# Kernel optimization log

Hardware: AMD Instinct MI355X
Metric: run time of the kernel (lower is better)

Reference implementation:

```python
import jax, jax.numpy as jnp
import numpy as np

N_ENTITIES = 100000
N_RELATIONS = 100
EMB = 64         # entity embedding_size
REL_DIM = 64     # relation_dim
BATCH = 65536


def setup_inputs() -> dict:
    key = jax.random.key(0)
    k1, k2, k3, k4, k5, k6 = jax.random.split(key, 6)
    head = jax.random.randint(k1, (BATCH,), 0, N_ENTITIES)
    relation = jax.random.randint(k2, (BATCH,), 0, N_RELATIONS)
    tail = jax.random.randint(k3, (BATCH,), 0, N_ENTITIES)
    entity_emb = jax.random.normal(k4, (N_ENTITIES, EMB), dtype=jnp.float32)
    relation_emb = jax.random.normal(k5, (N_RELATIONS, REL_DIM), dtype=jnp.float32)
    proj_emb = jax.random.normal(k6, (N_RELATIONS, EMB * REL_DIM), dtype=jnp.float32)
    return {
        "head": head,
        "relation": relation,
        "tail": tail,
        "entity_emb": entity_emb,
        "relation_emb": relation_emb,
        "proj_emb": proj_emb,
    }


def reference(head, relation, tail, entity_emb, relation_emb, proj_emb):
    h_emb = entity_emb[head]                           # [B, E]
    t_emb = entity_emb[tail]                           # [B, E]
    r_emb = relation_emb[relation]                     # [B, R]
    proj = proj_emb[relation].reshape(-1, EMB, REL_DIM)  # [B, E, R]
    h_proj = jnp.einsum('be,ber->br', h_emb, proj)     # [B, R]
    t_proj = jnp.einsum('be,ber->br', t_emb, proj)     # [B, R]
    diff = h_proj + r_emb - t_proj
    score = jnp.sum(diff * diff, axis=1)               # [B]
    return score
```

## Files before the change

kernel.cpp:

```cpp
#include <hip/hip_runtime.h>

#define BATCH   65536
#define NREL    100
#define NBB     64
#define NTILE   16

typedef __attribute__((ext_vector_type(8))) short bf16x8;
typedef __attribute__((ext_vector_type(4))) float f32x4;

__device__ __forceinline__ unsigned short f2bf(float x) {
    unsigned u = __float_as_uint(x);
    u += 0x7fffu + ((u >> 16) & 1u);
    return (unsigned short)(u >> 16);
}

__launch_bounds__(256)
__global__ void transr_bucket(const int* __restrict__ relation,
                              int* __restrict__ ws_hist,
                              int* __restrict__ ws_lpfx,
                              int* __restrict__ ws_bucket) {
    __shared__ int hist[NREL];
    __shared__ int scan[128];
    const int tid = threadIdx.x, bid = blockIdx.x;

    for (int r = tid; r < NREL; r += 256) hist[r] = 0;
    __syncthreads();

    const int4 v = ((const int4*)relation)[bid * 256 + tid];
    const int vals[4] = {v.x, v.y, v.z, v.w};
    int lr[4];
    #pragma unroll
    for (int k = 0; k < 4; ++k) lr[k] = atomicAdd(&hist[vals[k]], 1);
    __syncthreads();

    if (tid < 128) scan[tid] = (tid < NREL) ? hist[tid] : 0;
    __syncthreads();
    #pragma unroll
    for (int off = 1; off < 128; off <<= 1) {
        int t = 0;
        if (tid < 128 && tid >= off) t = scan[tid - off];
        __syncthreads();
        if (tid < 128) scan[tid] += t;
        __syncthreads();
    }

    const int i0 = (bid * 256 + tid) * 4;
    #pragma unroll
    for (int k = 0; k < 4; ++k) {
        const int rel = vals[k];
        ws_bucket[bid * 1024 + (scan[rel] - hist[rel]) + lr[k]] = i0 + k;
    }
    for (int r = tid; r < NREL; r += 256) {
        ws_hist[r * NBB + bid] = hist[r];
        ws_lpfx[r * NBB + bid] = scan[r] - hist[r];
    }
}

__launch_bounds__(256)
__global__ void transr_compute(const int* __restrict__ head,
                               const int* __restrict__ tail,
                               const float* __restrict__ ent,
                               const float* __restrict__ remb,
                               const float* __restrict__ proj,
                               const int* __restrict__ ws_hist,
                               const int* __restrict__ ws_lpfx,
                               const int* __restrict__ ws_bucket,
                               float* __restrict__ out) {
    __shared__ unsigned short Abuf[64 * 64];
    __shared__ unsigned short Bbuf[64 * 64];
    __shared__ float remb_s[64];
    __shared__ int   pfx_s[64];
    __shared__ int   lpfx_s[64];
    __shared__ int   bidx_s[64];
    __shared__ int   cnt_s;

    const int tid   = threadIdx.x;
    const int wid   = tid >> 6;
    const int lane  = tid & 63;
    const int rel   = blockIdx.y;
    const int start = blockIdx.x << 6;

    if (wid == 0) {
        int h = ws_hist[rel * NBB + lane];
        lpfx_s[lane] = ws_lpfx[rel * NBB + lane];
        const int own = h;
        #pragma unroll
        for (int m = 1; m < 64; m <<= 1) {
            int t = __shfl_up(h, m);
            if (lane >= m) h += t;
        }
        pfx_s[lane] = h - own;
        if (lane == 63) cnt_s = h;
    }

    {
        const int k = tid >> 2, q = tid & 3;
        const float4* p4 = (const float4*)(proj + (size_t)rel * 4096 + k * 64 + q * 16);
        const int khi = k >> 3, klo = k & 7;
        #pragma unroll
        for (int m = 0; m < 4; ++m) {
            float4 v = p4[m];
            const float vv[4] = {v.x, v.y, v.z, v.w};
            #pragma unroll
            for (int j2 = 0; j2 < 4; ++j2) {
                const int n = q * 16 + m * 4 + j2;
                Bbuf[n * 64 + ((khi ^ (n & 7)) * 8) + klo] = f2bf(vv[j2]);
            }
        }
    }
    if (tid < 64) remb_s[tid] = remb[rel * 64 + tid];
    __syncthreads();

    const int cnt = cnt_s;
    if (start >= cnt) return;

    {
        const int row = tid >> 2, q = tid & 3;
        const int j  = start + row;
        const int jj = (j < cnt) ? j : (cnt - 1);
        int lo = 0;
        #pragma unroll
        for (int s = 32; s; s >>= 1) {
            const int c = lo + s;
            if (c < 64 && pfx_s[c] <= jj) lo = c;
        }
        const int b = ws_bucket[lo * 1024 + lpfx_s[lo] + (jj - pfx_s[lo])];
        if (q == 0) bidx_s[row] = b;
        const int h = head[b], t = tail[b];
        const float4* h4 = (const float4*)(ent + (size_t)h * 64) + q * 4;
        const float4* t4 = (const float4*)(ent + (size_t)t * 64) + q * 4;
        #pragma unroll
        for (int i = 0; i < 2; ++i) {
            unsigned short u[8];
            #pragma unroll
            for (int m = 0; m < 2; ++m) {
                float4 a = h4[i * 2 + m], c = t4[i * 2 + m];
                u[m * 4 + 0] = f2bf(a.x - c.x);
                u[m * 4 + 1] = f2bf(a.y - c.y);
                u[m * 4 + 2] = f2bf(a.z - c.z);
                u[m * 4 + 3] = f2bf(a.w - c.w);
            }
            const int slice = (q * 2 + i) ^ (row & 7);
            *(bf16x8*)&Abuf[row * 64 + slice * 8] = *(bf16x8*)u;
        }
    }
    __syncthreads();

    const int arow = wid * 16 + (lane & 15);
    const int g    = lane >> 4;

    f32x4 acc[4];
    #pragma unroll
    for (int f = 0; f < 4; ++f) {
        const float rv = remb_s[f * 16 + (lane & 15)];
        acc[f] = (f32x4){rv, rv, rv, rv};
    }
    #pragma unroll
    for (int s = 0; s < 2; ++s) {
        const int ks = g + s * 4;
        bf16x8 av = *(const bf16x8*)&Abuf[arow * 64 + ((ks ^ (arow & 7)) * 8)];
        #pragma unroll
        for (int f = 0; f < 4; ++f) {
            const int col = f * 16 + (lane & 15);
            bf16x8 bv = *(const bf16x8*)&Bbuf[col * 64 + ((ks ^ (col & 7)) * 8)];
            acc[f] = __builtin_amdgcn_mfma_f32_16x16x32_bf16(av, bv, acc[f], 0, 0, 0);
        }
    }

    float ps[4];
    #pragma unroll
    for (int r = 0; r < 4; ++r)
        ps[r] = acc[0][r] * acc[0][r] + acc[1][r] * acc[1][r] +
                acc[2][r] * acc[2][r] + acc[3][r] * acc[3][r];
    #pragma unroll
    for (int m = 1; m < 16; m <<= 1) {
        #pragma unroll
        for (int r = 0; r < 4; ++r) ps[r] += __shfl_xor(ps[r], m, 64);
    }
    if ((lane & 15) == 0) {
        const int rowb = wid * 16 + g * 4;
        #pragma unroll
        for (int r = 0; r < 4; ++r) {
            const int j = start + rowb + r;
            if (j < cnt) out[bidx_s[rowb + r]] = ps[r];
        }
    }
}

extern "C" void kernel_launch(void* const* d_in, const int* in_sizes, int n_in,
                              void* d_out, int out_size, void* d_ws, size_t ws_size,
                              hipStream_t stream) {
    const int*   head     = (const int*)d_in[0];
    const int*   relation = (const int*)d_in[1];
    const int*   tail     = (const int*)d_in[2];
    const float* ent      = (const float*)d_in[3];
    const float* remb     = (const float*)d_in[4];
    const float* proj     = (const float*)d_in[5];
    float*       out      = (float*)d_out;

    int* ws_hist   = (int*)d_ws;
    int* ws_lpfx   = (int*)d_ws + 8192;
    int* ws_bucket = (int*)d_ws + 16384;

    transr_bucket<<<NBB, 256, 0, stream>>>(relation, ws_hist, ws_lpfx, ws_bucket);
    transr_compute<<<dim3(NTILE, NREL), 256, 0, stream>>>(
        head, tail, ent, remb, proj, ws_hist, ws_lpfx, ws_bucket, out);
}
```

Before: 22.72 us.

## Precompute bf16 swizzled projection matrices in prep kernel, copy into LDS in compute

```diff
diff --git a/kernel.cpp b/kernel.cpp
--- a/kernel.cpp
+++ b/kernel.cpp
@@ -15,44 +15,63 @@
 }
 
 __launch_bounds__(256)
-__global__ void transr_bucket(const int* __restrict__ relation,
-                              int* __restrict__ ws_hist,
-                              int* __restrict__ ws_lpfx,
-                              int* __restrict__ ws_bucket) {
-    __shared__ int hist[NREL];
-    __shared__ int scan[128];
+__global__ void transr_prep(const int* __restrict__ relation,
+                            const float* __restrict__ proj,
+                            int* __restrict__ ws_hist,
+                            int* __restrict__ ws_lpfx,
+                            int* __restrict__ ws_bucket,
+                            unsigned short* __restrict__ ws_pbf) {
     const int tid = threadIdx.x, bid = blockIdx.x;
 
-    for (int r = tid; r < NREL; r += 256) hist[r] = 0;
-    __syncthreads();
-
-    const int4 v = ((const int4*)relation)[bid * 256 + tid];
-    const int vals[4] = {v.x, v.y, v.z, v.w};
-    int lr[4];
-    #pragma unroll
-    for (int k = 0; k < 4; ++k) lr[k] = atomicAdd(&hist[vals[k]], 1);
-    __syncthreads();
-
-    if (tid < 128) scan[tid] = (tid < NREL) ? hist[tid] : 0;
-    __syncthreads();
-    #pragma unroll
-    for (int off = 1; off < 128; off <<= 1) {
-        int t = 0;
-        if (tid < 128 && tid >= off) t = scan[tid - off];
+    if (bid < NBB) {
+        __shared__ int hist[NREL];
+        __shared__ int scan[128];
+
+        for (int r = tid; r < NREL; r += 256) hist[r] = 0;
         __syncthreads();
-        if (tid < 128) scan[tid] += t;
+
+        const int4 v = ((const int4*)relation)[bid * 256 + tid];
+        const int vals[4] = {v.x, v.y, v.z, v.w};
+        int lr[4];
+        #pragma unroll
+        for (int k = 0; k < 4; ++k) lr[k] = atomicAdd(&hist[vals[k]], 1);
         __syncthreads();
-    }
-
-    const int i0 = (bid * 256 + tid) * 4;
-    #pragma unroll
-    for (int k = 0; k < 4; ++k) {
-        const int rel = vals[k];
-        ws_bucket[bid * 1024 + (scan[rel] - hist[rel]) + lr[k]] = i0 + k;
-    }
-    for (int r = tid; r < NREL; r += 256) {
-        ws_hist[r * NBB + bid] = hist[r];
-        ws_lpfx[r * NBB + bid] = scan[r] - hist[r];
+
+        if (tid < 128) scan[tid] = (tid < NREL) ? hist[tid] : 0;
+        __syncthreads();
+        #pragma unroll
+        for (int off = 1; off < 128; off <<= 1) {
+            int t = 0;
+            if (tid < 128 && tid >= off) t = scan[tid - off];
+            __syncthreads();
+            if (tid < 128) scan[tid] += t;
+            __syncthreads();
+        }
+
+        const int i0 = (bid * 256 + tid) * 4;
+        #pragma unroll
+        for (int k = 0; k < 4; ++k) {
+            const int rel = vals[k];
+            ws_bucket[bid * 1024 + (scan[rel] - hist[rel]) + lr[k]] = i0 + k;
+        }
+        for (int r = tid; r < NREL; r += 256) {
+            ws_hist[r * NBB + bid] = hist[r];
+            ws_lpfx[r * NBB + bid] = scan[r] - hist[r];
+        }
+    } else {
+        const int rel = bid - NBB;
+        const int n = tid >> 2, q = tid & 3;
+        const float* Pr = proj + (size_t)rel * 4096;
+        unsigned short* dst = ws_pbf + (size_t)rel * 4096;
+        #pragma unroll
+        for (int kh = 0; kh < 2; ++kh) {
+            const int khi = q * 2 + kh;
+            unsigned short u[8];
+            #pragma unroll
+            for (int klo = 0; klo < 8; ++klo)
+                u[klo] = f2bf(Pr[(khi * 8 + klo) * 64 + n]);
+            *(bf16x8*)&dst[n * 64 + ((khi ^ (n & 7)) << 3)] = *(bf16x8*)u;
+        }
     }
 }
 
@@ -61,10 +80,10 @@
                                const int* __restrict__ tail,
                                const float* __restrict__ ent,
                                const float* __restrict__ remb,
-                               const float* __restrict__ proj,
                                const int* __restrict__ ws_hist,
                                const int* __restrict__ ws_lpfx,
                                const int* __restrict__ ws_bucket,
+                               const unsigned short* __restrict__ ws_pbf,
                                float* __restrict__ out) {
     __shared__ unsigned short Abuf[64 * 64];
     __shared__ unsigned short Bbuf[64 * 64];
@@ -91,22 +110,6 @@
         }
         pfx_s[lane] = h - own;
         if (lane == 63) cnt_s = h;
-    }
-
-    {
-        const int k = tid >> 2, q = tid & 3;
-        const float4* p4 = (const float4*)(proj + (size_t)rel * 4096 + k * 64 + q * 16);
-        const int khi = k >> 3, klo = k & 7;
-        #pragma unroll
-        for (int m = 0; m < 4; ++m) {
-            float4 v = p4[m];
-            const float vv[4] = {v.x, v.y, v.z, v.w};
-            #pragma unroll
-            for (int j2 = 0; j2 < 4; ++j2) {
-                const int n = q * 16 + m * 4 + j2;
-                Bbuf[n * 64 + ((khi ^ (n & 7)) * 8) + klo] = f2bf(vv[j2]);
-            }
-        }
     }
     if (tid < 64) remb_s[tid] = remb[rel * 64 + tid];
     __syncthreads();
@@ -144,6 +147,12 @@
             *(bf16x8*)&Abuf[row * 64 + slice * 8] = *(bf16x8*)u;
         }
     }
+    {
+        const uint4* src = (const uint4*)(ws_pbf + (size_t)rel * 4096) + tid * 2;
+        uint4* dst = (uint4*)Bbuf + tid * 2;
+        dst[0] = src[0];
+        dst[1] = src[1];
+    }
     __syncthreads();
 
     const int arow = wid * 16 + (lane & 15);
@@ -201,8 +210,11 @@
     int* ws_hist   = (int*)d_ws;
     int* ws_lpfx   = (int*)d_ws + 8192;
     int* ws_bucket = (int*)d_ws + 16384;
-
-    transr_bucket<<<NBB, 256, 0, stream>>>(relation, ws_hist, ws_lpfx, ws_bucket);
+    unsigned short* ws_pbf =
+        (unsigned short*)((char*)d_ws + 512 * 1024);
+
+    transr_prep<<<NBB + NREL, 256, 0, stream>>>(relation, proj,
+                                                ws_hist, ws_lpfx, ws_bucket, ws_pbf);
     transr_compute<<<dim3(NTILE, NREL), 256, 0, stream>>>(
-        head, tail, ent, remb, proj, ws_hist, ws_lpfx, ws_bucket, out);
-}
+        head, tail, ent, remb, ws_hist, ws_lpfx, ws_bucket, ws_pbf, out);
+}
```

New measurement: 21.05 us. 1.08x faster.
